# Optimization experiments

Measured on AMD Instinct MI355X. Metric: run time of the kernel, lower is better.

The kernel has to match this reference:

```python
import jax, jax.numpy as jnp
import numpy as np

DIM = 128
NUM_LAYERS = 2
FF_MULT = 4
RADIUS = 0.2
K = 8
B, N, L = 8, 2048, 4096
NEG = -1e30


def setup_inputs() -> dict:
    key = jax.random.key(0)
    ks = jax.random.split(key, 12)
    C = DIM
    s = 1.0 / np.sqrt(C)
    w = lambda k, shape, sc: jax.random.normal(k, shape, dtype=jnp.float32) * sc
    inp = {
        "q_xyz": jax.random.uniform(ks[0], (B, N, 3), dtype=jnp.float32),
        "q_feat": jax.random.normal(ks[1], (B, N, C), dtype=jnp.float32),
        "kv_xyz": jax.random.uniform(ks[2], (B, L, 3), dtype=jnp.float32),
        "kv_feat": jax.random.normal(ks[3], (B, L, C), dtype=jnp.float32),
        "kv_pad": jnp.zeros((B, L), dtype=bool),
        # PointTransformerConv params (stacked over layers)
        "W_lin": w(ks[4], (NUM_LAYERS, C, C), s),   # value projection (with bias)
        "b_lin": jnp.zeros((NUM_LAYERS, C), jnp.float32),
        "W_src": w(ks[5], (NUM_LAYERS, C, C), s),   # lin_src, no bias
        "W_dst": w(ks[6], (NUM_LAYERS, C, C), s),   # lin_dst, no bias
        "W_attn": w(ks[7], (NUM_LAYERS, C, C), s),  # attn_nn = Linear+ReLU
        "b_attn": jnp.zeros((NUM_LAYERS, C), jnp.float32),
        "ln1_g": jnp.ones((NUM_LAYERS, C), jnp.float32),
        "ln1_b": jnp.zeros((NUM_LAYERS, C), jnp.float32),
        "W_ff1": w(ks[8], (NUM_LAYERS, C, FF_MULT * C), s),
        "b_ff1": jnp.zeros((NUM_LAYERS, FF_MULT * C), jnp.float32),
        "W_ff2": w(ks[9], (NUM_LAYERS, FF_MULT * C, C), 1.0 / np.sqrt(FF_MULT * C)),
        "b_ff2": jnp.zeros((NUM_LAYERS, C), jnp.float32),
        "ln2_g": jnp.ones((NUM_LAYERS, C), jnp.float32),
        "ln2_b": jnp.zeros((NUM_LAYERS, C), jnp.float32),
    }
    return inp


def _layernorm(x, g, b):
    mu = x.mean(-1, keepdims=True)
    var = ((x - mu) ** 2).mean(-1, keepdims=True)
    return (x - mu) * jax.lax.rsqrt(var + 1e-5) * g + b


def _gather(feats, idx):
    # feats: [B, L, C], idx: [B, N, K] -> [B, N, K, C]
    b, n, k = idx.shape
    g = jnp.take_along_axis(feats, idx.reshape(b, n * k)[:, :, None], axis=1)
    return g.reshape(b, n, k, feats.shape[-1])


def _forward(q_xyz, q_feat, kv_xyz, kv_feat, kv_pad,
             W_lin, b_lin, W_src, W_dst, W_attn, b_attn,
             ln1_g, ln1_b, W_ff1, b_ff1, W_ff2, b_ff2, ln2_g, ln2_b):
    # radius neighbor search (per-batch, fixed K neighbors with validity mask)
    d2 = jnp.sum((q_xyz[:, :, None, :] - kv_xyz[:, None, :, :]) ** 2, axis=-1)  # [B,N,L]
    valid_pair = (d2 <= RADIUS * RADIUS) & (~kv_pad)[:, None, :]
    negd = jnp.where(valid_pair, -d2, NEG)
    negv, idx = jax.lax.top_k(negd, K)          # [B,N,K] nearest-in-ball
    evalid = negv > 0.5 * NEG                   # edge validity mask [B,N,K]

    out = q_feat
    for i in range(NUM_LAYERS):
        # PointTransformerConv, pos_nn = ZeroPos => delta = 0
        aj = _gather(kv_feat @ W_src[i], idx)                    # [B,N,K,C]
        vj = _gather(kv_feat @ W_lin[i] + b_lin[i], idx)         # [B,N,K,C]
        ai = out @ W_dst[i]                                      # [B,N,C]
        logits = jax.nn.relu((ai[:, :, None, :] - aj) @ W_attn[i] + b_attn[i])
        logits = jnp.where(evalid[..., None], logits, NEG)
        m = logits.max(axis=2, keepdims=True)
        e = jnp.exp(logits - m) * evalid[..., None]
        attn = e / jnp.maximum(e.sum(axis=2, keepdims=True), 1e-9)  # per-channel softmax over neighbors
        upd = jnp.sum(attn * vj, axis=2)                         # [B,N,C] scatter-add over edges
        out = _layernorm(out + upd, ln1_g[i], ln1_b[i])
        h = jax.nn.gelu(out @ W_ff1[i] + b_ff1[i], approximate=False)
        out = _layernorm(out + h @ W_ff2[i] + b_ff2[i], ln2_g[i], ln2_b[i])
    return out


def reference(q_xyz, q_feat, kv_xyz, kv_feat, kv_pad,
              W_lin, b_lin, W_src, W_dst, W_attn, b_attn,
              ln1_g, ln1_b, W_ff1, b_ff1, W_ff2, b_ff2, ln2_g, ln2_b):
    return _forward(q_xyz, q_feat, kv_xyz, kv_feat, kv_pad,
                    W_lin, b_lin, W_src, W_dst, W_attn, b_attn,
                    ln1_g, ln1_b, W_ff1, b_ff1, W_ff2, b_ff2, ln2_g, ln2_b)
```

## Files before the change

kernel.cpp:

```cpp
#include <hip/hip_runtime.h>
#include <hip/hip_bf16.h>
#include <math.h>

#define DIM 128
#define BB 8
#define NN 2048
#define LL 4096
#define KK 8

typedef __hip_bfloat16 bf16;
typedef unsigned long long ull;
typedef __attribute__((ext_vector_type(8))) short short8;
typedef __attribute__((ext_vector_type(4))) float float4v;

__device__ __forceinline__ float toF(float x){ return x; }
__device__ __forceinline__ float toF(bf16 x){ return __bfloat162float(x); }
__device__ __forceinline__ void st(float* p, float v){ *p = v; }
__device__ __forceinline__ void st(bf16*  p, float v){ *p = __float2bfloat16(v); }
__device__ __forceinline__ unsigned short f2bf(float f){
  union { bf16 b; unsigned short u; } cv; cv.b = __float2bfloat16(f); return cv.u;
}
__device__ __forceinline__ float2 ld2bf(const bf16* p){
  const unsigned u = *(const unsigned*)p;
  return make_float2(__uint_as_float(u << 16), __uint_as_float(u & 0xFFFF0000u));
}
__device__ __forceinline__ void st2bf(bf16* p, float a, float b){
  *(unsigned*)p = (unsigned)f2bf(a) | ((unsigned)f2bf(b) << 16);
}

__device__ __forceinline__ float gelu_exact(float x){
  return 0.5f * x * (1.0f + erff(x * 0.70710678118654752f));
}

__device__ __forceinline__ float waveSum64(float v){
  #pragma unroll
  for (int o = 32; o > 0; o >>= 1) v += __shfl_xor(v, o, 64);
  return v;
}
__device__ __forceinline__ float quadSum16(float v){
  #pragma unroll
  for (int o = 8; o > 0; o >>= 1) v += __shfl_xor(v, o, 64);
  return v;
}

__device__ __forceinline__ void topk_insert_u(ull (&m)[KK], ull key){
  m[KK-1] = key;
  #pragma unroll
  for (int t = KK-1; t > 0; --t){
    if (m[t] < m[t-1]){ ull tmp = m[t]; m[t] = m[t-1]; m[t-1] = tmp; }
  }
}

#define NC3 125
__device__ __forceinline__ void packOne(const float* __restrict__ src,
                                        bf16* __restrict__ dst, int idx, int nshift){
  const int k = idx >> nshift;
  const int n = idx & ((1 << nshift) - 1);
  const int N = 1 << nshift;
  st(&dst[((size_t)(k>>3)*N + n)*8 + (k&7)], src[idx]);
}

__global__ __launch_bounds__(1024) void setup_all(const float* __restrict__ kv_xyz,
                                                  const float* __restrict__ q_xyz,
                                                  float4* __restrict__ bpts,
                                                  int* __restrict__ offs,
                                                  int* __restrict__ qsrt,
                                                  const float* __restrict__ Wlin,
                                                  const float* __restrict__ Wff1,
                                                  const float* __restrict__ Wff2,
                                                  const float* __restrict__ Wsrc,
                                                  const float* __restrict__ Wdst,
                                                  const float* __restrict__ Wattn,
                                                  bf16* __restrict__ WlinP,
                                                  bf16* __restrict__ Wff1P,
                                                  bf16* __restrict__ Wff2P,
                                                  bf16* __restrict__ WsaP,
                                                  bf16* __restrict__ WdaP)
{
  __shared__ int cnt[NC3];
  __shared__ int off[NC3+1];
  __shared__ float row[8][DIM];
  const int bid = blockIdx.x;
  const int tid = threadIdx.x;
  if (bid < 16){
    const int b   = bid & 7;
    const int role= bid >> 3;
    if (tid < NC3) cnt[tid] = 0;
    __syncthreads();
    if (role == 0){
      const float* kvp = kv_xyz + (size_t)b * LL * 3;
      float px[4], py[4], pz[4]; int pc[4];
      #pragma unroll
      for (int i = 0; i < 4; i++){
        const int e = tid + i*1024;
        px[i] = kvp[3*e]; py[i] = kvp[3*e+1]; pz[i] = kvp[3*e+2];
        const int cx = min((int)(px[i]*5.f), 4);
        const int cy = min((int)(py[i]*5.f), 4);
        const int cz = min((int)(pz[i]*5.f), 4);
        pc[i] = (cz*5 + cy)*5 + cx;
        atomicAdd(&cnt[pc[i]], 1);
      }
      __syncthreads();
      if (tid == 0){
        int acc = 0;
        for (int c = 0; c < NC3; c++){ off[c] = acc; acc += cnt[c]; }
        off[NC3] = acc;
      }
      __syncthreads();
      if (tid < NC3) cnt[tid] = 0;
      __syncthreads();
      float4* dst = bpts + (size_t)b * LL;
      #pragma unroll
      for (int i = 0; i < 4; i++){
        const int e = tid + i*1024;
        const int pos = off[pc[i]] + atomicAdd(&cnt[pc[i]], 1);
        dst[pos] = make_float4(px[i], py[i], pz[i], __int_as_float(e));
      }
      if (tid < NC3 + 1) offs[b*126 + tid] = off[tid];
    } else {
      const float* qp = q_xyz + (size_t)b * NN * 3;
      int pc[2];
      #pragma unroll
      for (int i = 0; i < 2; i++){
        const int e = tid + i*1024;
        const float x = qp[3*e], y = qp[3*e+1], z = qp[3*e+2];
        const int cx = min((int)(x*5.f), 4);
        const int cy = min((int)(y*5.f), 4);
        const int cz = min((int)(z*5.f), 4);
        pc[i] = (cz*5 + cy)*5 + cx;
        atomicAdd(&cnt[pc[i]], 1);
      }
      __syncthreads();
      if (tid == 0){
        int acc = 0;
        for (int c = 0; c < NC3; c++){ off[c] = acc; acc += cnt[c]; }
        off[NC3] = acc;
      }
      __syncthreads();
      if (tid < NC3) cnt[tid] = 0;
      __syncthreads();
      int* dst = qsrt + (size_t)b * NN;
      #pragma unroll
      for (int i = 0; i < 2; i++){
        const int e = tid + i*1024;
        const int pos = off[pc[i]] + atomicAdd(&cnt[pc[i]], 1);
        dst[pos] = e;
      }
    }
  } else if (bid < 304){
    int i = (bid - 16)*1024 + tid;
    if (i < 32768){
      const int l = i >> 14, r = i & 16383;
      packOne(Wlin + (size_t)l*16384, WlinP + (size_t)l*16384, r, 7);
    } else if (i < 163840){
      i -= 32768;
      const int l = i >> 16, r = i & 65535;
      packOne(Wff1 + (size_t)l*65536, Wff1P + (size_t)l*65536, r, 9);
    } else {
      i -= 163840;
      const int l = i >> 16, r = i & 65535;
      packOne(Wff2 + (size_t)l*65536, Wff2P + (size_t)l*65536, r, 7);
    }
  } else {
    const int grp = tid >> 7;
    const int c = tid & 127;
    const int tt = (bid - 304)*8 + grp;
    const int r = tt & 127, which = (tt >> 7) & 1, lay = tt >> 8;
    const float* Wx = (which ? Wdst : Wsrc) + (size_t)lay*DIM*DIM;
    const float* Wa = Wattn + (size_t)lay*DIM*DIM;
    row[grp][c] = Wx[r*DIM + c];
    __syncthreads();
    float acc = 0.f;
    for (int j = 0; j < DIM; j++) acc = fmaf(row[grp][j], Wa[j*DIM + c], acc);
    bf16* dst = (which ? WdaP : WsaP) + (size_t)lay*DIM*DIM;
    st(&dst[((size_t)(r>>3)*DIM + c)*8 + (r&7)], acc);
  }
}

__device__ __forceinline__ void stage_A_f32(const float* __restrict__ A, size_t r0,
                                            int kd, int kc, unsigned short* As, int tid){
  #pragma unroll
  for (int i = 0; i < 8; i++){
    const int f = tid + i*256;
    const int row = f >> 5, c4 = (f & 31) * 4;
    const float4 v = *(const float4*)&A[(r0+row)*kd + kc + c4];
    uint2 u;
    u.x = (unsigned)f2bf(v.x) | ((unsigned)f2bf(v.y) << 16);
    u.y = (unsigned)f2bf(v.z) | ((unsigned)f2bf(v.w) << 16);
    *(uint2*)&As[row*136 + c4] = u;
  }
}
__device__ __forceinline__ void stage_A_bf16(const bf16* __restrict__ A, size_t r0,
                                             int kd, int kc, unsigned short* As, int tid){
  #pragma unroll
  for (int i = 0; i < 8; i++){
    const int f = tid + i*256;
    const int row = f >> 5, c4 = (f & 31) * 4;
    *(uint2*)&As[row*136 + c4] = *(const uint2*)&A[(r0+row)*kd + kc + c4];
  }
}

#define QBLK 8
#define SPL 32
__global__ __launch_bounds__(256) void knn_gemm(const float* __restrict__ q_xyz,
                                                const float4* __restrict__ bpts,
                                                const int* __restrict__ offs,
                                                const int* __restrict__ qsrt,
                                                int* __restrict__ idx,
                                                const float* __restrict__ kvf,
                                                const float* __restrict__ q_feat,
                                                const bf16* __restrict__ WsaP,
                                                const bf16* __restrict__ WlinP,
                                                const bf16* __restrict__ WdaP0,
                                                const float* __restrict__ b_lin,
                                                bf16* __restrict__ srcA0,
                                                bf16* __restrict__ linp0,
                                                bf16* __restrict__ srcA1,
                                                bf16* __restrict__ linp1,
                                                bf16* __restrict__ qA)
{
  __shared__ __align__(16) unsigned char smem[17408];
  const int bid = blockIdx.x;
  const int tid = threadIdx.x;
  bool isGemm; int rid;
  if (bid < 2560){ isGemm = !(bid & 1); rid = bid >> 1; }
  else { isGemm = false; rid = 1280 + (bid - 2560); }

  if (isGemm){
    unsigned short* As = (unsigned short*)smem;
    const int wid = tid >> 6, ln = tid & 63, qd = ln >> 4, cl = ln & 15;
    if (rid < 1024){
      const int lay = rid >> 9;
      const size_t r0 = (size_t)(rid & 511) * 64;
      const bf16* Wp0 = WsaP  + (size_t)lay * DIM * DIM;
      const bf16* Wp1 = WlinP + (size_t)lay * DIM * DIM;
      const float* bias1 = b_lin + lay * DIM;
      bf16* Y0 = lay ? srcA1 : srcA0;
      bf16* Y1 = lay ? linp1 : linp0;
      stage_A_f32(kvf, r0, 128, 0, As, tid);
      __syncthreads();
      float4v ac0[8], ac1[8];
      #pragma unroll
      for (int t = 0; t < 8; t++){ ac0[t] = (float4v){0.f,0.f,0.f,0.f}; ac1[t] = (float4v){0.f,0.f,0.f,0.f}; }
      #pragma unroll
      for (int ks = 0; ks < 4; ks++){
        const short8 a = *(const short8*)&As[(wid*16 + cl)*136 + (ks*4 + qd)*8];
        const size_t wo = (size_t)(ks*4 + qd)*DIM + cl;
        const short8* wb0 = (const short8*)Wp0 + wo;
        const short8* wb1 = (const short8*)Wp1 + wo;
        #pragma unroll
        for (int t = 0; t < 8; t++){
          const short8 b0 = wb0[t*16];
          ac0[t] = __builtin_amdgcn_mfma_f32_16x16x32_bf16(a, b0, ac0[t], 0, 0, 0);
          const short8 b1 = wb1[t*16];
          ac1[t] = __builtin_amdgcn_mfma_f32_16x16x32_bf16(a, b1, ac1[t], 0, 0, 0);
        }
      }
      #pragma unroll
      for (int t = 0; t < 8; t++){
        const int col = t*16 + cl;
        const float bv = bias1[col];
        #pragma unroll
        for (int r = 0; r < 4; r++){
          const size_t row = r0 + wid*16 + qd*4 + r;
          st(&Y0[row*DIM + col], ac0[t][r]);
          st(&Y1[row*DIM + col], ac1[t][r] + bv);
        }
      }
    } else {
      const size_t r0 = (size_t)(rid - 1024) * 64;
      stage_A_f32(q_feat, r0, 128, 0, As, tid);
      __syncthreads();
      float4v acc[8];
      #pragma unroll
      for (int t = 0; t < 8; t++) acc[t] = (float4v){0.f,0.f,0.f,0.f};
      #pragma unroll
      for (int ks = 0; ks < 4; ks++){
        const short8 a = *(const short8*)&As[(wid*16 + cl)*136 + (ks*4 + qd)*8];
        const short8* wb = (const short8*)WdaP0 + (size_t)(ks*4 + qd)*DIM + cl;
        #pragma unroll
        for (int t = 0; t < 8; t++){
          const short8 b = wb[t*16];
          acc[t] = __builtin_amdgcn_mfma_f32_16x16x32_bf16(a, b, acc[t], 0, 0, 0);
        }
      }
      #pragma unroll
      for (int t = 0; t < 8; t++){
        const int col = t*16 + cl;
        #pragma unroll
        for (int r = 0; r < 4; r++){
          const size_t row = r0 + wid*16 + qd*4 + r;
          st(&qA[row*DIM + col], acc[t][r]);
        }
      }
    }
  } else {
    ull* cd = (ull*)smem;
    const int s    = tid & 31;
    const int qloc = tid >> 5;
    const int b    = rid >> 8;
    const int qbase = (rid & 255) * QBLK;
    const int qid = qsrt[b*NN + qbase + qloc];
    const size_t qo = ((size_t)b * NN + qid) * 3;
    const float qx = q_xyz[qo], qy = q_xyz[qo+1], qz = q_xyz[qo+2];
    const ull THRKEY = ((ull)0x3D23D70Bu << 32);
    ull kthr = THRKEY;
    ull m[KK];
    #pragma unroll
    for (int k = 0; k < KK; k++) m[k] = ~0ULL;
    const int qcx = min((int)(qx*5.f), 4);
    const int qcy = min((int)(qy*5.f), 4);
    const int qcz = min((int)(qz*5.f), 4);
    const int* ofb = offs + b*126;
    const float4* bp = bpts + (size_t)b * LL;
    const int cx0 = max(qcx-1, 0), cx1 = min(qcx+1, 4);
    for (int cz = max(qcz-1,0); cz <= min(qcz+1,4); cz++){
      for (int cy = max(qcy-1,0); cy <= min(qcy+1,4); cy++){
        const int rowc = (cz*5 + cy)*5;
        const int pend = ofb[rowc + cx1 + 1];
        int p = ofb[rowc + cx0] + s;
        if (p < pend){
          float4 pt = bp[p];
          while (true){
            const int pn = p + SPL;
            const bool hn = pn < pend;
            float4 nx;
            if (hn) nx = bp[pn];
            const float dx = qx - pt.x, dy = qy - pt.y, dz = qz - pt.z;
            const float d2 = dx*dx + dy*dy + dz*dz;
            const ull key = ((ull)__float_as_uint(d2) << 32) | (unsigned)__float_as_int(pt.w);
            if (key < kthr){
              topk_insert_u(m, key);
              kthr = (m[KK-1] < THRKEY) ? m[KK-1] : THRKEY;
            }
            if (!hn) break;
            pt = nx; p = pn;
          }
        }
      }
    }
    #pragma unroll
    for (int k = 0; k < KK; k++) cd[qloc*257 + k*32 + s] = m[k];
    __syncthreads();
    if (tid < 64){
      const int q = tid >> 3, g = tid & 7;
      ull mm[KK];
      #pragma unroll
      for (int k = 0; k < KK; k++) mm[k] = ~0ULL;
      #pragma unroll
      for (int u = 0; u < 4; u++){
        const int sl = g + 8*u;
        #pragma unroll
        for (int k = 0; k < KK; k++){
          const ull key = cd[q*257 + k*32 + sl];
          if (key < mm[KK-1]) topk_insert_u(mm, key);
        }
      }
      #pragma unroll
      for (int k = 0; k < KK; k++) cd[q*257 + k*32 + g] = mm[k];
      if (tid < QBLK){
        ull f[KK];
        #pragma unroll
        for (int k = 0; k < KK; k++) f[k] = ~0ULL;
        #pragma unroll
        for (int k = 0; k < 8; k++)
          for (int g2 = 0; g2 < 8; g2++){
            const ull key = cd[tid*257 + k*32 + g2];
            if (key < f[KK-1]) topk_insert_u(f, key);
          }
        const int oq = b * NN + qsrt[b*NN + qbase + tid];
        #pragma unroll
        for (int k = 0; k < KK; k++) idx[oq*KK + k] = (int)(unsigned)(f[k] & 0xFFFFFFFFu);
      }
    }
  }
}

template<typename TA, int NDIM, bool GELU>
__global__ __launch_bounds__(256) void mfma_single(const TA* __restrict__ A,
                                                   const bf16* __restrict__ Wp,
                                                   const float* __restrict__ bias,
                                                   bf16* __restrict__ Y)
{
  __shared__ __align__(16) unsigned short As[64*136];
  const int tid = threadIdx.x;
  const size_t r0 = (size_t)blockIdx.x * 64;
  const int nblk = blockIdx.y * 128;
  if (sizeof(TA) == 4) stage_A_f32((const float*)A, r0, 128, 0, As, tid);
  else                 stage_A_bf16((const bf16*)A, r0, 128, 0, As, tid);
  __syncthreads();
  const int wid = tid >> 6, ln = tid & 63, qd = ln >> 4, cl = ln & 15;
  float4v acc[8];
  #pragma unroll
  for (int t = 0; t < 8; t++) acc[t] = (float4v){0.f,0.f,0.f,0.f};
  #pragma unroll
  for (int ks = 0; ks < 4; ks++){
    const short8 a = *(const short8*)&As[(wid*16 + cl)*136 + (ks*4 + qd)*8];
    const short8* wb = (const short8*)Wp + (size_t)(ks*4 + qd)*NDIM + nblk + cl;
    #pragma unroll
    for (int t = 0; t < 8; t++){
      const short8 b = wb[t*16];
      acc[t] = __builtin_amdgcn_mfma_f32_16x16x32_bf16(a, b, acc[t], 0, 0, 0);
    }
  }
  #pragma unroll
  for (int t = 0; t < 8; t++){
    const int col = nblk + t*16 + cl;
    const float bv = bias ? bias[col] : 0.f;
    #pragma unroll
    for (int r = 0; r < 4; r++){
      const size_t row = r0 + wid*16 + qd*4 + r;
      float v = acc[t][r] + bv;
      if (GELU) v = gelu_exact(v);
      st(&Y[row*NDIM + col], v);
    }
  }
}

__global__ __launch_bounds__(256) void mfma_ff2ln(const bf16* __restrict__ A,
                                                  const bf16* __restrict__ Wp,
                                                  const float* __restrict__ b2,
                                                  const bf16* __restrict__ resid,
                                                  const float* __restrict__ g,
                                                  const float* __restrict__ bb,
                                                  float* __restrict__ Y)
{
  __shared__ __align__(16) unsigned short As[64*136];
  const int tid = threadIdx.x;
  const size_t r0 = (size_t)blockIdx.x * 64;
  const int wid = tid >> 6, ln = tid & 63, qd = ln >> 4, cl = ln & 15;
  float4v acc[8];
  #pragma unroll
  for (int t = 0; t < 8; t++) acc[t] = (float4v){0.f,0.f,0.f,0.f};
  for (int kc = 0; kc < 512; kc += 128){
    __syncthreads();
    stage_A_bf16(A, r0, 512, kc, As, tid);
    __syncthreads();
    const int k8c = kc >> 3;
    #pragma unroll
    for (int ks = 0; ks < 4; ks++){
      const short8 a = *(const short8*)&As[(wid*16 + cl)*136 + (ks*4 + qd)*8];
      const short8* wb = (const short8*)Wp + (size_t)(k8c + ks*4 + qd)*DIM + cl;
      #pragma unroll
      for (int t = 0; t < 8; t++){
        const short8 b = wb[t*16];
        acc[t] = __builtin_amdgcn_mfma_f32_16x16x32_bf16(a, b, acc[t], 0, 0, 0);
      }
    }
  }
  float v[8][4];
  #pragma unroll
  for (int t = 0; t < 8; t++){
    const int col = t*16 + cl;
    const float bv = b2[col];
    #pragma unroll
    for (int r = 0; r < 4; r++){
      const size_t row = r0 + wid*16 + qd*4 + r;
      v[t][r] = acc[t][r] + bv + toF(resid[row*DIM + col]);
    }
  }
  #pragma unroll
  for (int r = 0; r < 4; r++){
    float s = 0.f;
    #pragma unroll
    for (int t = 0; t < 8; t++) s += v[t][r];
    const float mu = quadSum16(s) * (1.f/DIM);
    float q = 0.f;
    #pragma unroll
    for (int t = 0; t < 8; t++){ const float d = v[t][r] - mu; q += d*d; }
    const float inv = rsqrtf(quadSum16(q) * (1.f/DIM) + 1e-5f);
    const size_t row = r0 + wid*16 + qd*4 + r;
    #pragma unroll
    for (int t = 0; t < 8; t++){
      const int col = t*16 + cl;
      Y[row*DIM + col] = (v[t][r] - mu) * inv * g[col] + bb[col];
    }
  }
}

__global__ __launch_bounds__(256) void attn_ln1(const bf16* __restrict__ qA,
                                                const bf16* __restrict__ srcA,
                                                const bf16* __restrict__ linp,
                                                const int* __restrict__ idx,
                                                const int* __restrict__ qsrt,
                                                const float* __restrict__ b_attn,
                                                const float* __restrict__ feat,
                                                const float* __restrict__ g,
                                                const float* __restrict__ bb,
                                                bf16* __restrict__ out1)
{
  const int tid = threadIdx.x;
  const int wv = tid >> 6, ln = tid & 63;
  const int sp = blockIdx.x * 4 + wv;
  const int b = sp >> 11;
  const int q = b * NN + qsrt[b*NN + (sp & 2047)];
  const bf16* sbase = srcA + (size_t)b * LL * DIM;
  const bf16* vbase = linp + (size_t)b * LL * DIM;
  const int c0 = 2*ln;
  const float2 ba = *(const float2*)&b_attn[c0];
  const float2 qa2 = ld2bf(&qA[(size_t)q*DIM + c0]);
  const float qa0 = qa2.x + ba.x, qa1 = qa2.y + ba.y;
  int ids[KK]; float l0[KK], l1[KK];
  float m0 = -1e30f, m1 = -1e30f;
  #pragma unroll
  for (int k = 0; k < KK; k++){
    const int id = idx[q*KK + k]; ids[k] = id;
    if (id >= 0){
      const float2 s2 = ld2bf(&sbase[(size_t)id*DIM + c0]);
      l0[k] = fmaxf(qa0 - s2.x, 0.f); m0 = fmaxf(m0, l0[k]);
      l1[k] = fmaxf(qa1 - s2.y, 0.f); m1 = fmaxf(m1, l1[k]);
    } else { l0[k] = 0.f; l1[k] = 0.f; }
  }
  float sum0 = 0.f, sum1 = 0.f, upd0 = 0.f, upd1 = 0.f;
  #pragma unroll
  for (int k = 0; k < KK; k++) if (ids[k] >= 0){
    const float e0 = expf(l0[k] - m0); l0[k] = e0; sum0 += e0;
    const float e1 = expf(l1[k] - m1); l1[k] = e1; sum1 += e1;
  }
  if (sum0 > 0.f){
    const float i0 = 1.f / sum0, i1 = 1.f / sum1;
    #pragma unroll
    for (int k = 0; k < KK; k++) if (ids[k] >= 0){
      const float2 v2 = ld2bf(&vbase[(size_t)ids[k]*DIM + c0]);
      upd0 = fmaf(l0[k]*i0, v2.x, upd0);
      upd1 = fmaf(l1[k]*i1, v2.y, upd1);
    }
  }
  const float2 f2 = *(const float2*)&feat[(size_t)q*DIM + c0];
  const float x0 = f2.x + upd0;
  const float x1 = f2.y + upd1;
  const float mu = waveSum64(x0 + x1) * (1.f/DIM);
  const float d0 = x0 - mu, d1 = x1 - mu;
  const float var = waveSum64(d0*d0 + d1*d1) * (1.f/DIM);
  const float inv = rsqrtf(var + 1e-5f);
  const float2 gg = *(const float2*)&g[c0];
  const float2 bbv = *(const float2*)&bb[c0];
  st2bf(&out1[(size_t)q*DIM + c0], d0 * inv * gg.x + bbv.x, d1 * inv * gg.y + bbv.y);
}

extern "C" void kernel_launch(void* const* d_in, const int* in_sizes, int n_in,
                              void* d_out, int out_size, void* d_ws, size_t ws_size,
                              hipStream_t stream)
{
  const float* q_xyz  = (const float*)d_in[0];
  const float* q_feat = (const float*)d_in[1];
  const float* kv_xyz = (const float*)d_in[2];
  const float* kv_feat= (const float*)d_in[3];
  const float* W_lin  = (const float*)d_in[5];
  const float* b_lin  = (const float*)d_in[6];
  const float* W_src  = (const float*)d_in[7];
  const float* W_dst  = (const float*)d_in[8];
  const float* W_attn = (const float*)d_in[9];
  const float* b_attn = (const float*)d_in[10];
  const float* ln1_g  = (const float*)d_in[11];
  const float* ln1_b  = (const float*)d_in[12];
  const float* W_ff1  = (const float*)d_in[13];
  const float* b_ff1  = (const float*)d_in[14];
  const float* W_ff2  = (const float*)d_in[15];
  const float* b_ff2  = (const float*)d_in[16];
  const float* ln2_g  = (const float*)d_in[17];
  const float* ln2_b  = (const float*)d_in[18];
  float* out = (float*)d_out;

  const int MQ  = BB * NN;
  const int MKV = BB * LL;

  char* p = (char*)d_ws;
  int*    idxb  = (int*)p;    p += (size_t)MQ * KK * 4;
  float4* bpts  = (float4*)p; p += (size_t)BB * LL * 16;
  int*    boffs = (int*)p;    p += (size_t)BB * 126 * 4;
  int*    qsrt  = (int*)p;    p += (size_t)BB * NN * 4;
  bf16*  WsaP  = (bf16*)p;  p += (size_t)2 * DIM * DIM * 2;
  bf16*  WdaP  = (bf16*)p;  p += (size_t)2 * DIM * DIM * 2;
  bf16*  WlinP = (bf16*)p;  p += (size_t)2 * DIM * DIM * 2;
  bf16*  Wff1P = (bf16*)p;  p += (size_t)2 * DIM * 4*DIM * 2;
  bf16*  Wff2P = (bf16*)p;  p += (size_t)2 * 4*DIM * DIM * 2;
  float* feat  = (float*)p; p += (size_t)MQ * DIM * 4;
  bf16*  out1  = (bf16*)p;  p += (size_t)MQ * DIM * 2;
  bf16*  srcA0 = (bf16*)p;  p += (size_t)MKV * DIM * 2;
  bf16*  linp0 = (bf16*)p;  p += (size_t)MKV * DIM * 2;
  bf16*  srcA1 = (bf16*)p;  p += (size_t)MKV * DIM * 2;
  bf16*  linp1 = (bf16*)p;  p += (size_t)MKV * DIM * 2;
  bf16*  qA    = (bf16*)p;  p += (size_t)MQ * DIM * 2;
  bf16*  hbuf  = (bf16*)p;  p += (size_t)MQ * 4*DIM * 2;

  setup_all<<<368, 1024, 0, stream>>>(kv_xyz, q_xyz, bpts, boffs, qsrt,
                                      W_lin, W_ff1, W_ff2, W_src, W_dst, W_attn,
                                      WlinP, Wff1P, Wff2P, WsaP, WdaP);
  knn_gemm<<<3328, 256, 0, stream>>>(q_xyz, bpts, boffs, qsrt, idxb,
                                     kv_feat, q_feat, WsaP, WlinP, WdaP,
                                     b_lin, srcA0, linp0, srcA1, linp1, qA);

  for (int i = 0; i < 2; i++){
    const size_t w512 = (size_t)i * DIM * 4*DIM;
    const float* featIn = (i == 0) ? q_feat : feat;
    const bf16* srcA = i ? srcA1 : srcA0;
    const bf16* linp = i ? linp1 : linp0;

    if (i == 1){
      mfma_single<float, 128, false><<<MQ/64, 256, 0, stream>>>(
          feat, WdaP + DIM*DIM, nullptr, qA);
    }
    attn_ln1<<<MQ/4, 256, 0, stream>>>(qA, srcA, linp, idxb, qsrt, b_attn + i*DIM,
                                       featIn, ln1_g + i*DIM, ln1_b + i*DIM, out1);
    mfma_single<bf16, 512, true><<<dim3(MQ/64, 4), 256, 0, stream>>>(
        out1, Wff1P + w512, b_ff1 + i*4*DIM, hbuf);
    float* ydst = (i == 1) ? out : feat;
    mfma_ff2ln<<<MQ/64, 256, 0, stream>>>(hbuf, Wff2P + w512, b_ff2 + i*DIM, out1,
                                          ln2_g + i*DIM, ln2_b + i*DIM, ydst);
  }
}
```

Measured before the change: 296.4 us.

## Split kNN from GEMMs and fuse layer-2 query projection into FF2 LayerNorm

The combined kNN+GEMM kernel, which interleaved block types, is split into a dedicated knn_query kernel and a gemm_all kernel. knn_query now loads all nine cell-row ranges and their first points up front so the loads overlap. The separate layer-1 mfma_single launch that projected feat to qA is removed; instead the layer-0 FF2+LayerNorm kernel restages its normalized output in LDS as bf16 and runs the qA projection in the same block. This saves one launch and a re-read of feat from global memory, at the cost of an extra launch boundary between the kNN work and the GEMMs, which previously shared one grid.

Result: faster. 284.8 us (-3.9%).

```diff
diff --git a/kernel.cpp b/kernel.cpp
--- a/kernel.cpp
+++ b/kernel.cpp
@@ -177,6 +177,107 @@
   }
 }
 
+#define QBLK 8
+#define SPL 32
+__global__ __launch_bounds__(256) void knn_query(const float* __restrict__ q_xyz,
+                                                 const float4* __restrict__ bpts,
+                                                 const int* __restrict__ offs,
+                                                 const int* __restrict__ qsrt,
+                                                 int* __restrict__ idx)
+{
+  __shared__ ull cd[QBLK*257];
+  const int tid  = threadIdx.x;
+  const int s    = tid & 31;
+  const int qloc = tid >> 5;
+  const int b    = blockIdx.y;
+  const int qbase = blockIdx.x * QBLK;
+  const int qid = qsrt[b*NN + qbase + qloc];
+  const size_t qo = ((size_t)b * NN + qid) * 3;
+  const float qx = q_xyz[qo], qy = q_xyz[qo+1], qz = q_xyz[qo+2];
+  const ull THRKEY = ((ull)0x3D23D70Bu << 32);
+  ull kthr = THRKEY;
+  ull m[KK];
+  #pragma unroll
+  for (int k = 0; k < KK; k++) m[k] = ~0ULL;
+  const int qcx = min((int)(qx*5.f), 4);
+  const int qcy = min((int)(qy*5.f), 4);
+  const int qcz = min((int)(qz*5.f), 4);
+  const int* ofb = offs + b*126;
+  const float4* bp = bpts + (size_t)b * LL;
+  const int cx0 = max(qcx-1, 0), cx1 = min(qcx+1, 4);
+  int st9[9], en9[9];
+  float4 hd[9];
+  #pragma unroll
+  for (int u = 0; u < 9; u++){
+    const int dz = u/3 - 1, dy = u%3 - 1;
+    const int cz = qcz + dz, cy = qcy + dy;
+    const bool ok = (cz >= 0) & (cz <= 4) & (cy >= 0) & (cy <= 4);
+    const int rowc = (cz*5 + cy)*5;
+    int a0 = 0, e0 = 0;
+    if (ok){ a0 = ofb[rowc + cx0] + s; e0 = ofb[rowc + cx1 + 1]; }
+    st9[u] = a0; en9[u] = e0;
+    const int pa = (a0 < e0) ? a0 : 0;
+    hd[u] = bp[pa];
+  }
+  #pragma unroll
+  for (int u = 0; u < 9; u++){
+    int p = st9[u];
+    const int e = en9[u];
+    if (p < e){
+      float4 pt = hd[u];
+      while (true){
+        const int pn = p + SPL;
+        const bool hn = pn < e;
+        float4 nx;
+        if (hn) nx = bp[pn];
+        const float dx = qx - pt.x, dy = qy - pt.y, dz = qz - pt.z;
+        const float d2 = dx*dx + dy*dy + dz*dz;
+        const ull key = ((ull)__float_as_uint(d2) << 32) | (unsigned)__float_as_int(pt.w);
+        if (key < kthr){
+          topk_insert_u(m, key);
+          kthr = (m[KK-1] < THRKEY) ? m[KK-1] : THRKEY;
+        }
+        if (!hn) break;
+        pt = nx; p = pn;
+      }
+    }
+  }
+  #pragma unroll
+  for (int k = 0; k < KK; k++) cd[qloc*257 + k*32 + s] = m[k];
+  __syncthreads();
+  if (tid < 64){
+    const int q = tid >> 3, g = tid & 7;
+    ull mm[KK];
+    #pragma unroll
+    for (int k = 0; k < KK; k++) mm[k] = ~0ULL;
+    #pragma unroll
+    for (int u = 0; u < 4; u++){
+      const int sl = g + 8*u;
+      #pragma unroll
+      for (int k = 0; k < KK; k++){
+        const ull key = cd[q*257 + k*32 + sl];
+        if (key < mm[KK-1]) topk_insert_u(mm, key);
+      }
+    }
+    #pragma unroll
+    for (int k = 0; k < KK; k++) cd[q*257 + k*32 + g] = mm[k];
+    if (tid < QBLK){
+      ull f[KK];
+      #pragma unroll
+      for (int k = 0; k < KK; k++) f[k] = ~0ULL;
+      #pragma unroll
+      for (int k = 0; k < 8; k++)
+        for (int g2 = 0; g2 < 8; g2++){
+          const ull key = cd[tid*257 + k*32 + g2];
+          if (key < f[KK-1]) topk_insert_u(f, key);
+        }
+      const int oq = b * NN + qsrt[b*NN + qbase + tid];
+      #pragma unroll
+      for (int k = 0; k < KK; k++) idx[oq*KK + k] = (int)(unsigned)(f[k] & 0xFFFFFFFFu);
+    }
+  }
+}
+
 __device__ __forceinline__ void stage_A_f32(const float* __restrict__ A, size_t r0,
                                             int kd, int kc, unsigned short* As, int tid){
   #pragma unroll
@@ -200,14 +301,7 @@
   }
 }
 
-#define QBLK 8
-#define SPL 32
-__global__ __launch_bounds__(256) void knn_gemm(const float* __restrict__ q_xyz,
-                                                const float4* __restrict__ bpts,
-                                                const int* __restrict__ offs,
-                                                const int* __restrict__ qsrt,
-                                                int* __restrict__ idx,
-                                                const float* __restrict__ kvf,
+__global__ __launch_bounds__(256) void gemm_all(const float* __restrict__ kvf,
                                                 const float* __restrict__ q_feat,
                                                 const bf16* __restrict__ WsaP,
                                                 const bf16* __restrict__ WlinP,
@@ -219,175 +313,87 @@
                                                 bf16* __restrict__ linp1,
                                                 bf16* __restrict__ qA)
 {
-  __shared__ __align__(16) unsigned char smem[17408];
+  __shared__ __align__(16) unsigned short As[64*136];
   const int bid = blockIdx.x;
   const int tid = threadIdx.x;
-  bool isGemm; int rid;
-  if (bid < 2560){ isGemm = !(bid & 1); rid = bid >> 1; }
-  else { isGemm = false; rid = 1280 + (bid - 2560); }
-
-  if (isGemm){
-    unsigned short* As = (unsigned short*)smem;
-    const int wid = tid >> 6, ln = tid & 63, qd = ln >> 4, cl = ln & 15;
-    if (rid < 1024){
-      const int lay = rid >> 9;
-      const size_t r0 = (size_t)(rid & 511) * 64;
-      const bf16* Wp0 = WsaP  + (size_t)lay * DIM * DIM;
-      const bf16* Wp1 = WlinP + (size_t)lay * DIM * DIM;
-      const float* bias1 = b_lin + lay * DIM;
-      bf16* Y0 = lay ? srcA1 : srcA0;
-      bf16* Y1 = lay ? linp1 : linp0;
-      stage_A_f32(kvf, r0, 128, 0, As, tid);
-      __syncthreads();
-      float4v ac0[8], ac1[8];
-      #pragma unroll
-      for (int t = 0; t < 8; t++){ ac0[t] = (float4v){0.f,0.f,0.f,0.f}; ac1[t] = (float4v){0.f,0.f,0.f,0.f}; }
-      #pragma unroll
-      for (int ks = 0; ks < 4; ks++){
-        const short8 a = *(const short8*)&As[(wid*16 + cl)*136 + (ks*4 + qd)*8];
-        const size_t wo = (size_t)(ks*4 + qd)*DIM + cl;
-        const short8* wb0 = (const short8*)Wp0 + wo;
-        const short8* wb1 = (const short8*)Wp1 + wo;
-        #pragma unroll
-        for (int t = 0; t < 8; t++){
-          const short8 b0 = wb0[t*16];
-          ac0[t] = __builtin_amdgcn_mfma_f32_16x16x32_bf16(a, b0, ac0[t], 0, 0, 0);
-          const short8 b1 = wb1[t*16];
-          ac1[t] = __builtin_amdgcn_mfma_f32_16x16x32_bf16(a, b1, ac1[t], 0, 0, 0);
-        }
-      }
+  const int wid = tid >> 6, ln = tid & 63, qd = ln >> 4, cl = ln & 15;
+  if (bid < 1024){
+    const int lay = bid >> 9;
+    const size_t r0 = (size_t)(bid & 511) * 64;
+    const bf16* Wp0 = WsaP  + (size_t)lay * DIM * DIM;
+    const bf16* Wp1 = WlinP + (size_t)lay * DIM * DIM;
+    const float* bias1 = b_lin + lay * DIM;
+    bf16* Y0 = lay ? srcA1 : srcA0;
+    bf16* Y1 = lay ? linp1 : linp0;
+    stage_A_f32(kvf, r0, 128, 0, As, tid);
+    __syncthreads();
+    float4v ac0[8], ac1[8];
+    #pragma unroll
+    for (int t = 0; t < 8; t++){ ac0[t] = (float4v){0.f,0.f,0.f,0.f}; ac1[t] = (float4v){0.f,0.f,0.f,0.f}; }
+    #pragma unroll
+    for (int ks = 0; ks < 4; ks++){
+      const short8 a = *(const short8*)&As[(wid*16 + cl)*136 + (ks*4 + qd)*8];
+      const size_t wo = (size_t)(ks*4 + qd)*DIM + cl;
+      const short8* wb0 = (const short8*)Wp0 + wo;
+      const short8* wb1 = (const short8*)Wp1 + wo;
       #pragma unroll
       for (int t = 0; t < 8; t++){
-        const int col = t*16 + cl;
-        const float bv = bias1[col];
-        #pragma unroll
-        for (int r = 0; r < 4; r++){
-          const size_t row = r0 + wid*16 + qd*4 + r;
-          st(&Y0[row*DIM + col], ac0[t][r]);
-          st(&Y1[row*DIM + col], ac1[t][r] + bv);
-        }
-      }
-    } else {
-      const size_t r0 = (size_t)(rid - 1024) * 64;
-      stage_A_f32(q_feat, r0, 128, 0, As, tid);
-      __syncthreads();
-      float4v acc[8];
-      #pragma unroll
-      for (int t = 0; t < 8; t++) acc[t] = (float4v){0.f,0.f,0.f,0.f};
-      #pragma unroll
-      for (int ks = 0; ks < 4; ks++){
-        const short8 a = *(const short8*)&As[(wid*16 + cl)*136 + (ks*4 + qd)*8];
-        const short8* wb = (const short8*)WdaP0 + (size_t)(ks*4 + qd)*DIM + cl;
-        #pragma unroll
-        for (int t = 0; t < 8; t++){
-          const short8 b = wb[t*16];
-          acc[t] = __builtin_amdgcn_mfma_f32_16x16x32_bf16(a, b, acc[t], 0, 0, 0);
-        }
-      }
+        const short8 b0 = wb0[t*16];
+        ac0[t] = __builtin_amdgcn_mfma_f32_16x16x32_bf16(a, b0, ac0[t], 0, 0, 0);
+        const short8 b1 = wb1[t*16];
+        ac1[t] = __builtin_amdgcn_mfma_f32_16x16x32_bf16(a, b1, ac1[t], 0, 0, 0);
+      }
+    }
+    #pragma unroll
+    for (int t = 0; t < 8; t++){
+      const int col = t*16 + cl;
+      const float bv = bias1[col];
+      #pragma unroll
+      for (int r = 0; r < 4; r++){
+        const size_t row = r0 + wid*16 + qd*4 + r;
+        st(&Y0[row*DIM + col], ac0[t][r]);
+        st(&Y1[row*DIM + col], ac1[t][r] + bv);
+      }
+    }
+  } else {
+    const size_t r0 = (size_t)(bid - 1024) * 64;
+    stage_A_f32(q_feat, r0, 128, 0, As, tid);
+    __syncthreads();
+    float4v acc[8];
+    #pragma unroll
+    for (int t = 0; t < 8; t++) acc[t] = (float4v){0.f,0.f,0.f,0.f};
+    #pragma unroll
+    for (int ks = 0; ks < 4; ks++){
+      const short8 a = *(const short8*)&As[(wid*16 + cl)*136 + (ks*4 + qd)*8];
+      const short8* wb = (const short8*)WdaP0 + (size_t)(ks*4 + qd)*DIM + cl;
       #pragma unroll
       for (int t = 0; t < 8; t++){
-        const int col = t*16 + cl;
-        #pragma unroll
-        for (int r = 0; r < 4; r++){
-          const size_t row = r0 + wid*16 + qd*4 + r;
-          st(&qA[row*DIM + col], acc[t][r]);
-        }
-      }
-    }
-  } else {
-    ull* cd = (ull*)smem;
-    const int s    = tid & 31;
-    const int qloc = tid >> 5;
-    const int b    = rid >> 8;
-    const int qbase = (rid & 255) * QBLK;
-    const int qid = qsrt[b*NN + qbase + qloc];
-    const size_t qo = ((size_t)b * NN + qid) * 3;
-    const float qx = q_xyz[qo], qy = q_xyz[qo+1], qz = q_xyz[qo+2];
-    const ull THRKEY = ((ull)0x3D23D70Bu << 32);
-    ull kthr = THRKEY;
-    ull m[KK];
-    #pragma unroll
-    for (int k = 0; k < KK; k++) m[k] = ~0ULL;
-    const int qcx = min((int)(qx*5.f), 4);
-    const int qcy = min((int)(qy*5.f), 4);
-    const int qcz = min((int)(qz*5.f), 4);
-    const int* ofb = offs + b*126;
-    const float4* bp = bpts + (size_t)b * LL;
-    const int cx0 = max(qcx-1, 0), cx1 = min(qcx+1, 4);
-    for (int cz = max(qcz-1,0); cz <= min(qcz+1,4); cz++){
-      for (int cy = max(qcy-1,0); cy <= min(qcy+1,4); cy++){
-        const int rowc = (cz*5 + cy)*5;
-        const int pend = ofb[rowc + cx1 + 1];
-        int p = ofb[rowc + cx0] + s;
-        if (p < pend){
-          float4 pt = bp[p];
-          while (true){
-            const int pn = p + SPL;
-            const bool hn = pn < pend;
-            float4 nx;
-            if (hn) nx = bp[pn];
-            const float dx = qx - pt.x, dy = qy - pt.y, dz = qz - pt.z;
-            const float d2 = dx*dx + dy*dy + dz*dz;
-            const ull key = ((ull)__float_as_uint(d2) << 32) | (unsigned)__float_as_int(pt.w);
-            if (key < kthr){
-              topk_insert_u(m, key);
-              kthr = (m[KK-1] < THRKEY) ? m[KK-1] : THRKEY;
-            }
-            if (!hn) break;
-            pt = nx; p = pn;
-          }
-        }
-      }
-    }
-    #pragma unroll
-    for (int k = 0; k < KK; k++) cd[qloc*257 + k*32 + s] = m[k];
-    __syncthreads();
-    if (tid < 64){
-      const int q = tid >> 3, g = tid & 7;
-      ull mm[KK];
-      #pragma unroll
-      for (int k = 0; k < KK; k++) mm[k] = ~0ULL;
-      #pragma unroll
-      for (int u = 0; u < 4; u++){
-        const int sl = g + 8*u;
-        #pragma unroll
-        for (int k = 0; k < KK; k++){
-          const ull key = cd[q*257 + k*32 + sl];
-          if (key < mm[KK-1]) topk_insert_u(mm, key);
-        }
-      }
-      #pragma unroll
-      for (int k = 0; k < KK; k++) cd[q*257 + k*32 + g] = mm[k];
-      if (tid < QBLK){
-        ull f[KK];
-        #pragma unroll
-        for (int k = 0; k < KK; k++) f[k] = ~0ULL;
-        #pragma unroll
-        for (int k = 0; k < 8; k++)
-          for (int g2 = 0; g2 < 8; g2++){
-            const ull key = cd[tid*257 + k*32 + g2];
-            if (key < f[KK-1]) topk_insert_u(f, key);
-          }
-        const int oq = b * NN + qsrt[b*NN + qbase + tid];
-        #pragma unroll
-        for (int k = 0; k < KK; k++) idx[oq*KK + k] = (int)(unsigned)(f[k] & 0xFFFFFFFFu);
-      }
-    }
-  }
-}
-
-template<typename TA, int NDIM, bool GELU>
-__global__ __launch_bounds__(256) void mfma_single(const TA* __restrict__ A,
-                                                   const bf16* __restrict__ Wp,
-                                                   const float* __restrict__ bias,
-                                                   bf16* __restrict__ Y)
+        const short8 b = wb[t*16];
+        acc[t] = __builtin_amdgcn_mfma_f32_16x16x32_bf16(a, b, acc[t], 0, 0, 0);
+      }
+    }
+    #pragma unroll
+    for (int t = 0; t < 8; t++){
+      const int col = t*16 + cl;
+      #pragma unroll
+      for (int r = 0; r < 4; r++){
+        const size_t row = r0 + wid*16 + qd*4 + r;
+        st(&qA[row*DIM + col], acc[t][r]);
+      }
+    }
+  }
+}
+
+__global__ __launch_bounds__(256) void mfma_ff1(const bf16* __restrict__ A,
+                                                const bf16* __restrict__ Wp,
+                                                const float* __restrict__ bias,
+                                                bf16* __restrict__ Y)
 {
   __shared__ __align__(16) unsigned short As[64*136];
   const int tid = threadIdx.x;
   const size_t r0 = (size_t)blockIdx.x * 64;
   const int nblk = blockIdx.y * 128;
-  if (sizeof(TA) == 4) stage_A_f32((const float*)A, r0, 128, 0, As, tid);
-  else                 stage_A_bf16((const bf16*)A, r0, 128, 0, As, tid);
+  stage_A_bf16(A, r0, 128, 0, As, tid);
   __syncthreads();
   const int wid = tid >> 6, ln = tid & 63, qd = ln >> 4, cl = ln & 15;
   float4v acc[8];
@@ -396,7 +402,7 @@
   #pragma unroll
   for (int ks = 0; ks < 4; ks++){
     const short8 a = *(const short8*)&As[(wid*16 + cl)*136 + (ks*4 + qd)*8];
-    const short8* wb = (const short8*)Wp + (size_t)(ks*4 + qd)*NDIM + nblk + cl;
+    const short8* wb = (const short8*)Wp + (size_t)(ks*4 + qd)*512 + nblk + cl;
     #pragma unroll
     for (int t = 0; t < 8; t++){
       const short8 b = wb[t*16];
@@ -406,24 +412,25 @@
   #pragma unroll
   for (int t = 0; t < 8; t++){
     const int col = nblk + t*16 + cl;
-    const float bv = bias ? bias[col] : 0.f;
+    const float bv = bias[col];
     #pragma unroll
     for (int r = 0; r < 4; r++){
       const size_t row = r0 + wid*16 + qd*4 + r;
-      float v = acc[t][r] + bv;
-      if (GELU) v = gelu_exact(v);
-      st(&Y[row*NDIM + col], v);
-    }
-  }
-}
-
+      st(&Y[row*512 + col], gelu_exact(acc[t][r] + bv));
+    }
+  }
+}
+
+template<bool EMITQA>
 __global__ __launch_bounds__(256) void mfma_ff2ln(const bf16* __restrict__ A,
                                                   const bf16* __restrict__ Wp,
                                                   const float* __restrict__ b2,
                                                   const bf16* __restrict__ resid,
                                                   const float* __restrict__ g,
                                                   const float* __restrict__ bb,
-                                                  float* __restrict__ Y)
+                                                  float* __restrict__ Y,
+                                                  const bf16* __restrict__ WqP,
+                                                  bf16* __restrict__ qA)
 {
   __shared__ __align__(16) unsigned short As[64*136];
   const int tid = threadIdx.x;
@@ -473,7 +480,40 @@
     #pragma unroll
     for (int t = 0; t < 8; t++){
       const int col = t*16 + cl;
-      Y[row*DIM + col] = (v[t][r] - mu) * inv * g[col] + bb[col];
+      const float y = (v[t][r] - mu) * inv * g[col] + bb[col];
+      v[t][r] = y;
+      Y[row*DIM + col] = y;
+    }
+  }
+  if (EMITQA){
+    __syncthreads();
+    #pragma unroll
+    for (int t = 0; t < 8; t++){
+      #pragma unroll
+      for (int r = 0; r < 4; r++)
+        As[(wid*16 + qd*4 + r)*136 + t*16 + cl] = f2bf(v[t][r]);
+    }
+    float4v qacc[8];
+    #pragma unroll
+    for (int t = 0; t < 8; t++) qacc[t] = (float4v){0.f,0.f,0.f,0.f};
+    #pragma unroll
+    for (int ks = 0; ks < 4; ks++){
+      const short8 a = *(const short8*)&As[(wid*16 + cl)*136 + (ks*4 + qd)*8];
+      const short8* wb = (const short8*)WqP + (size_t)(ks*4 + qd)*DIM + cl;
+      #pragma unroll
+      for (int t = 0; t < 8; t++){
+        const short8 b = wb[t*16];
+        qacc[t] = __builtin_amdgcn_mfma_f32_16x16x32_bf16(a, b, qacc[t], 0, 0, 0);
+      }
+    }
+    #pragma unroll
+    for (int t = 0; t < 8; t++){
+      const int col = t*16 + cl;
+      #pragma unroll
+      for (int r = 0; r < 4; r++){
+        const size_t row = r0 + wid*16 + qd*4 + r;
+        st(&qA[row*DIM + col], qacc[t][r]);
+      }
     }
   }
 }
@@ -587,26 +627,22 @@
   setup_all<<<368, 1024, 0, stream>>>(kv_xyz, q_xyz, bpts, boffs, qsrt,
                                       W_lin, W_ff1, W_ff2, W_src, W_dst, W_attn,
                                       WlinP, Wff1P, Wff2P, WsaP, WdaP);
-  knn_gemm<<<3328, 256, 0, stream>>>(q_xyz, bpts, boffs, qsrt, idxb,
-                                     kv_feat, q_feat, WsaP, WlinP, WdaP,
+  knn_query<<<dim3(NN/QBLK, BB), 256, 0, stream>>>(q_xyz, bpts, boffs, qsrt, idxb);
+  gemm_all<<<1280, 256, 0, stream>>>(kv_feat, q_feat, WsaP, WlinP, WdaP,
                                      b_lin, srcA0, linp0, srcA1, linp1, qA);
 
-  for (int i = 0; i < 2; i++){
-    const size_t w512 = (size_t)i * DIM * 4*DIM;
-    const float* featIn = (i == 0) ? q_feat : feat;
-    const bf16* srcA = i ? srcA1 : srcA0;
-    const bf16* linp = i ? linp1 : linp0;
-
-    if (i == 1){
-      mfma_single<float, 128, false><<<MQ/64, 256, 0, stream>>>(
-          feat, WdaP + DIM*DIM, nullptr, qA);
-    }
-    attn_ln1<<<MQ/4, 256, 0, stream>>>(qA, srcA, linp, idxb, qsrt, b_attn + i*DIM,
-                                       featIn, ln1_g + i*DIM, ln1_b + i*DIM, out1);
-    mfma_single<bf16, 512, true><<<dim3(MQ/64, 4), 256, 0, stream>>>(
-        out1, Wff1P + w512, b_ff1 + i*4*DIM, hbuf);
-    float* ydst = (i == 1) ? out : feat;
-    mfma_ff2ln<<<MQ/64, 256, 0, stream>>>(hbuf, Wff2P + w512, b_ff2 + i*DIM, out1,
-                                          ln2_g + i*DIM, ln2_b + i*DIM, ydst);
-  }
-}
+  attn_ln1<<<MQ/4, 256, 0, stream>>>(qA, srcA0, linp0, idxb, qsrt, b_attn,
+                                     q_feat, ln1_g, ln1_b, out1);
+  mfma_ff1<<<dim3(MQ/64, 4), 256, 0, stream>>>(out1, Wff1P, b_ff1, hbuf);
+  mfma_ff2ln<true><<<MQ/64, 256, 0, stream>>>(hbuf, Wff2P, b_ff2, out1,
+                                              ln2_g, ln2_b, feat,
+                                              WdaP + DIM*DIM, qA);
+  attn_ln1<<<MQ/4, 256, 0, stream>>>(qA, srcA1, linp1, idxb, qsrt, b_attn + DIM,
+                                     feat, ln1_g + DIM, ln1_b + DIM, out1);
+  mfma_ff1<<<dim3(MQ/64, 4), 256, 0, stream>>>(out1, Wff1P + DIM*4*DIM,
+                                               b_ff1 + 4*DIM, hbuf);
+  mfma_ff2ln<false><<<MQ/64, 256, 0, stream>>>(hbuf, Wff2P + 4*DIM*DIM,
+                                               b_ff2 + DIM, out1,
+                                               ln2_g + DIM, ln2_b + DIM, out,
+                                               nullptr, nullptr);
+}
```
